# Kernel tuning notes

Hardware: AMD Instinct MI355X
Metric: run time of the kernel (lower is better)

## Reference

```python
import jax, jax.numpy as jnp
import numpy as np

N_NODES = 100000


def gcn_layer(x, src, dst, W, b, num_nodes):
    """PyG GCNConv: out = D^-1/2 (A + I) D^-1/2 (x W) + b, with self-loops."""
    h = x @ W  # [N, out_dim]
    # add self-loops
    loop = jnp.arange(num_nodes, dtype=src.dtype)
    s = jnp.concatenate([src, loop])
    d = jnp.concatenate([dst, loop])
    # symmetric normalization (degree counted on destination, incl. self-loops)
    deg = jax.ops.segment_sum(jnp.ones_like(d, dtype=h.dtype), d, num_segments=num_nodes)
    dinv = jnp.where(deg > 0, jax.lax.rsqrt(deg), 0.0)
    norm = dinv[s] * dinv[d]  # [E+N]
    # gather -> weight -> scatter-add
    msg = h[s] * norm[:, None]  # [E+N, out_dim]
    out = jax.ops.segment_sum(msg, d, num_segments=num_nodes)
    return out + b


def setup_inputs() -> dict:
    key = jax.random.key(0)
    k1, k2, k3, k4 = jax.random.split(key, 4)
    in_chan, h1, h2 = 256, 128, 64
    n_edges = 1600000
    x = jax.random.normal(k1, (N_NODES, in_chan), dtype=jnp.float32)
    edge_index = jax.random.randint(k2, (2, n_edges), 0, N_NODES, dtype=jnp.int64)
    W1 = jax.random.normal(k3, (in_chan, h1), dtype=jnp.float32) * (1.0 / np.sqrt(in_chan))
    b1 = jnp.zeros((h1,), dtype=jnp.float32)
    W2 = jax.random.normal(k4, (h1, h2), dtype=jnp.float32) * (1.0 / np.sqrt(h1))
    b2 = jnp.zeros((h2,), dtype=jnp.float32)
    return {"x": x, "edge_index": edge_index, "W1": W1, "b1": b1, "W2": W2, "b2": b2}


def reference(x, edge_index, W1, b1, W2, b2):
    src, dst = edge_index[0], edge_index[1]
    h = jax.nn.relu(gcn_layer(x, src, dst, W1, b1, N_NODES))
    return jax.nn.relu(gcn_layer(h, src, dst, W2, b2, N_NODES))
```

## Files before the change

kernel.cpp:

```cpp
#include <hip/hip_runtime.h>
#include <hip/hip_fp16.h>

#define NNODES 100000

#define OFF_W1TH     0UL
#define OFF_W1TL     65536UL
#define OFF_W2TH     131072UL
#define OFF_W2TL     147456UL
#define OFF_BCNT     163840UL
#define OFF_BBASE    165888UL
#define OFF_BCUR     167936UL
#define OFF_ROWPTR   400128UL
#define OFF_DINV     1200640UL
#define OFF_COL      1605632UL
#define OFF_EBUF     8005632UL
#define OFF_H1G      8005632UL
#define OFF_H1OUT    59205632UL

typedef __attribute__((ext_vector_type(8))) short bf16x8;
typedef __attribute__((ext_vector_type(4))) float f32x4;

__device__ inline ushort f2bf(float f) {
    unsigned u = __float_as_uint(f);
    unsigned r = u + 0x7fffu + ((u >> 16) & 1u);
    return (ushort)(r >> 16);
}
__device__ inline float bf2f(ushort h) { return __uint_as_float(((unsigned)h) << 16); }

__global__ __launch_bounds__(256) void bincount(const int* __restrict__ dst,
                                                int* __restrict__ bcnt, int E) {
    __shared__ int lc[512];
    int t = threadIdx.x;
    lc[t] = 0; lc[t + 256] = 0;
    __syncthreads();
    for (int e = blockIdx.x * 256 + t; e < E; e += gridDim.x * 256)
        atomicAdd(&lc[dst[e] >> 8], 1);
    __syncthreads();
    if (lc[t]) atomicAdd(&bcnt[t], lc[t]);
    if (lc[t + 256]) atomicAdd(&bcnt[t + 256], lc[t + 256]);
}

__global__ __launch_bounds__(512) void bscan(const int* __restrict__ bcnt,
                                             int* __restrict__ bbase,
                                             int* __restrict__ bcur,
                                             int* __restrict__ rowptr,
                                             int NB, int N, int E) {
    __shared__ int s[512];
    int t = threadIdx.x;
    int v = (t < NB) ? bcnt[t] : 0;
    s[t] = v;
    __syncthreads();
    for (int off = 1; off < 512; off <<= 1) {
        int add = (t >= off) ? s[t - off] : 0;
        __syncthreads();
        s[t] += add;
        __syncthreads();
    }
    if (t < NB) {
        int ex = s[t] - v;
        bbase[t] = ex;
        bcur[t] = ex;
    }
    if (t == 0) rowptr[N] = E;
}

#define CHUNK 4096
__global__ __launch_bounds__(256) void binscatter(const int* __restrict__ src,
                                                  const int* __restrict__ dst,
                                                  int* __restrict__ bcur,
                                                  int2* __restrict__ ebuf, int E) {
    __shared__ int lc[512];
    __shared__ int gb[512];
    int t = threadIdx.x;
    lc[t] = 0; lc[t + 256] = 0;
    __syncthreads();
    int base = blockIdx.x * CHUNK;
    int rb[16];
#pragma unroll
    for (int i = 0; i < 16; ++i) {
        int e = base + i * 256 + t;
        if (e < E) {
            int b = dst[e] >> 8;
            rb[i] = (b << 12) | atomicAdd(&lc[b], 1);
        } else rb[i] = -1;
    }
    __syncthreads();
    if (lc[t]) gb[t] = atomicAdd(&bcur[t], lc[t]);
    if (lc[t + 256]) gb[t + 256] = atomicAdd(&bcur[t + 256], lc[t + 256]);
    __syncthreads();
#pragma unroll
    for (int i = 0; i < 16; ++i) {
        if (rb[i] >= 0) {
            int e = base + i * 256 + t;
            int b = rb[i] >> 12, r = rb[i] & 4095;
            ebuf[gb[b] + r] = make_int2(src[e], dst[e]);
        }
    }
}

__global__ __launch_bounds__(256) void buildcsr(const int2* __restrict__ ebuf,
                                                const int* __restrict__ bbase,
                                                const int* __restrict__ bcnt,
                                                int* __restrict__ rowptr,
                                                int* __restrict__ colarr,
                                                float* __restrict__ dinv, int N) {
    int b = blockIdx.x;
    int t = threadIdx.x;
    int start = bbase[b];
    int cnt = bcnt[b];
    int n0 = b << 8;
    __shared__ int nc[256];
    __shared__ int s[256];
    __shared__ int ncur[256];
    nc[t] = 0;
    __syncthreads();
    for (int e = t; e < cnt; e += 256) atomicAdd(&nc[ebuf[start + e].y - n0], 1);
    __syncthreads();
    int own = nc[t];
    s[t] = own;
    __syncthreads();
    for (int off = 1; off < 256; off <<= 1) {
        int add = (t >= off) ? s[t - off] : 0;
        __syncthreads();
        s[t] += add;
        __syncthreads();
    }
    int rowbase = start + s[t] - own;
    if (n0 + t < N) {
        rowptr[n0 + t] = rowbase;
        dinv[n0 + t] = rsqrtf((float)(own + 1));
    }
    ncur[t] = rowbase;
    __syncthreads();
    for (int e = t; e < cnt; e += 256) {
        int2 p = ebuf[start + e];
        int slot = atomicAdd(&ncur[p.y - n0], 1);
        colarr[slot] = p.x;
    }
}

__global__ __launch_bounds__(256) void split_wt(const float* __restrict__ W,
                                                ushort* __restrict__ hi,
                                                ushort* __restrict__ lo,
                                                int K, int N) {
    int idx = blockIdx.x * 256 + threadIdx.x;
    if (idx >= K * N) return;
    int k = idx / N, n = idx - k * N;
    float v = W[idx];
    ushort h = f2bf(v);
    float rest = v - bf2f(h);
    hi[(size_t)n * K + k] = h;
    lo[(size_t)n * K + k] = f2bf(rest);
}

template <int BN, int KTOT>
__global__ __launch_bounds__(256) void gemm_mfma(const float* __restrict__ A,
                                                 const ushort* __restrict__ Bh_g,
                                                 const ushort* __restrict__ Bl_g,
                                                 const float* __restrict__ dinv,
                                                 _Float16* __restrict__ C, int M) {
    constexpr int KC = 64;
    constexpr int LDK = KC + 8;
    __shared__ ushort Ah[128][LDK];
    __shared__ ushort Al[128][LDK];
    __shared__ ushort Bh[BN][LDK];
    __shared__ ushort Bl[BN][LDK];

    const int tid = threadIdx.x;
    const int wave = tid >> 6;
    const int lane = tid & 63;
    const int lm = lane & 15;
    const int q = lane >> 4;
    const int m0 = blockIdx.x * 128;

    constexpr int NT = BN / 16;
    f32x4 acc[2][NT];
#pragma unroll
    for (int a = 0; a < 2; ++a)
#pragma unroll
        for (int b = 0; b < NT; ++b) acc[a][b] = (f32x4){0.f, 0.f, 0.f, 0.f};

    for (int k0 = 0; k0 < KTOT; k0 += KC) {
#pragma unroll
        for (int i = 0; i < 8; ++i) {
            int v = tid + i * 256;
            int row = v >> 4;
            int kk = (v & 15) << 2;
            int gr = m0 + row;
            float4 val = make_float4(0.f, 0.f, 0.f, 0.f);
            if (gr < M) val = *(const float4*)&A[(size_t)gr * KTOT + k0 + kk];
            ushort h0 = f2bf(val.x), h1 = f2bf(val.y), h2 = f2bf(val.z), h3 = f2bf(val.w);
            *(ushort4*)&Ah[row][kk] = make_ushort4(h0, h1, h2, h3);
            *(ushort4*)&Al[row][kk] = make_ushort4(
                f2bf(val.x - bf2f(h0)), f2bf(val.y - bf2f(h1)),
                f2bf(val.z - bf2f(h2)), f2bf(val.w - bf2f(h3)));
        }
        constexpr int BV = BN * KC / 8 / 256;
#pragma unroll
        for (int i = 0; i < BV; ++i) {
            int v = tid + i * 256;
            int row = v >> 3;
            int kk = (v & 7) << 3;
            *(uint4*)&Bh[row][kk] = *(const uint4*)&Bh_g[(size_t)row * KTOT + k0 + kk];
            *(uint4*)&Bl[row][kk] = *(const uint4*)&Bl_g[(size_t)row * KTOT + k0 + kk];
        }
        __syncthreads();

#pragma unroll
        for (int ks = 0; ks < KC / 32; ++ks) {
            int kb = ks * 32 + q * 8;
            bf16x8 a_h[2], a_l[2];
#pragma unroll
            for (int mt = 0; mt < 2; ++mt) {
                int r = wave * 32 + mt * 16 + lm;
                a_h[mt] = *(const bf16x8*)&Ah[r][kb];
                a_l[mt] = *(const bf16x8*)&Al[r][kb];
            }
#pragma unroll
            for (int nt = 0; nt < NT; ++nt) {
                int c = nt * 16 + lm;
                bf16x8 b_h = *(const bf16x8*)&Bh[c][kb];
                bf16x8 b_l = *(const bf16x8*)&Bl[c][kb];
#pragma unroll
                for (int mt = 0; mt < 2; ++mt) {
                    acc[mt][nt] = __builtin_amdgcn_mfma_f32_16x16x32_bf16(a_h[mt], b_h, acc[mt][nt], 0, 0, 0);
                    acc[mt][nt] = __builtin_amdgcn_mfma_f32_16x16x32_bf16(a_h[mt], b_l, acc[mt][nt], 0, 0, 0);
                    acc[mt][nt] = __builtin_amdgcn_mfma_f32_16x16x32_bf16(a_l[mt], b_h, acc[mt][nt], 0, 0, 0);
                }
            }
        }
        __syncthreads();
    }

#pragma unroll
    for (int mt = 0; mt < 2; ++mt) {
#pragma unroll
        for (int i = 0; i < 4; ++i) {
            int r = m0 + wave * 32 + mt * 16 + q * 4 + i;
            if (r < M) {
                float dv = dinv[r];
#pragma unroll
                for (int nt = 0; nt < NT; ++nt) {
                    C[(size_t)r * BN + nt * 16 + lm] = (_Float16)(acc[mt][nt][i] * dv);
                }
            }
        }
    }
}

__global__ __launch_bounds__(256) void agg_f2h(const __half2* __restrict__ g,
                                               const int* __restrict__ rowptr,
                                               const int* __restrict__ colarr,
                                               const float* __restrict__ dinv,
                                               const float* __restrict__ bias,
                                               float2* __restrict__ out, int n) {
    int node = blockIdx.x * 4 + (threadIdx.x >> 6);
    int lane = threadIdx.x & 63;
    if (node >= n) return;
    int beg = rowptr[node];
    int end = rowptr[node + 1];
    float2 acc = __half22float2(g[(size_t)node * 64 + lane]);
    int p = beg;
    for (; p + 4 <= end; p += 4) {
        int s0 = colarr[p], s1 = colarr[p + 1], s2 = colarr[p + 2], s3 = colarr[p + 3];
        float2 v0 = __half22float2(g[(size_t)s0 * 64 + lane]);
        float2 v1 = __half22float2(g[(size_t)s1 * 64 + lane]);
        float2 v2 = __half22float2(g[(size_t)s2 * 64 + lane]);
        float2 v3 = __half22float2(g[(size_t)s3 * 64 + lane]);
        acc.x += (v0.x + v1.x) + (v2.x + v3.x);
        acc.y += (v0.y + v1.y) + (v2.y + v3.y);
    }
    for (; p < end; ++p) {
        float2 v = __half22float2(g[(size_t)colarr[p] * 64 + lane]);
        acc.x += v.x;
        acc.y += v.y;
    }
    float dv = dinv[node];
    float2 b = ((const float2*)bias)[lane];
    float2 o;
    o.x = fmaxf(fmaf(acc.x, dv, b.x), 0.f);
    o.y = fmaxf(fmaf(acc.y, dv, b.y), 0.f);
    out[(size_t)node * 64 + lane] = o;
}

__global__ __launch_bounds__(256) void agg_f1h(const _Float16* __restrict__ g,
                                               const int* __restrict__ rowptr,
                                               const int* __restrict__ colarr,
                                               const float* __restrict__ dinv,
                                               const float* __restrict__ bias,
                                               float* __restrict__ out, int n) {
    int node = blockIdx.x * 4 + (threadIdx.x >> 6);
    int lane = threadIdx.x & 63;
    if (node >= n) return;
    int beg = rowptr[node];
    int end = rowptr[node + 1];
    float acc = (float)g[(size_t)node * 64 + lane];
    int p = beg;
    for (; p + 4 <= end; p += 4) {
        int s0 = colarr[p], s1 = colarr[p + 1], s2 = colarr[p + 2], s3 = colarr[p + 3];
        float v0 = (float)g[(size_t)s0 * 64 + lane];
        float v1 = (float)g[(size_t)s1 * 64 + lane];
        float v2 = (float)g[(size_t)s2 * 64 + lane];
        float v3 = (float)g[(size_t)s3 * 64 + lane];
        acc += (v0 + v1) + (v2 + v3);
    }
    for (; p < end; ++p) acc += (float)g[(size_t)colarr[p] * 64 + lane];
    float dv = dinv[node];
    float o = fmaxf(fmaf(acc, dv, bias[lane]), 0.f);
    out[(size_t)node * 64 + lane] = o;
}

extern "C" void kernel_launch(void* const* d_in, const int* in_sizes, int n_in,
                              void* d_out, int out_size, void* d_ws, size_t ws_size,
                              hipStream_t stream) {
    const float* x  = (const float*)d_in[0];
    const int*   ei = (const int*)d_in[1];
    const float* W1 = (const float*)d_in[2];
    const float* b1 = (const float*)d_in[3];
    const float* W2 = (const float*)d_in[4];
    const float* b2 = (const float*)d_in[5];
    float* out = (float*)d_out;

    const int E = in_sizes[1] / 2;
    const int H1 = in_sizes[3];
    const int K1 = in_sizes[2] / H1;
    const int N = in_sizes[0] / K1;
    const int H2 = in_sizes[4] / H1;
    const int* src = ei;
    const int* dst = ei + E;
    const int NB = (N + 255) >> 8;

    char* ws = (char*)d_ws;
    ushort*   w1th   = (ushort*)(ws + OFF_W1TH);
    ushort*   w1tl   = (ushort*)(ws + OFF_W1TL);
    ushort*   w2th   = (ushort*)(ws + OFF_W2TH);
    ushort*   w2tl   = (ushort*)(ws + OFF_W2TL);
    int*      bcnt   = (int*)(ws + OFF_BCNT);
    int*      bbase  = (int*)(ws + OFF_BBASE);
    int*      bcur   = (int*)(ws + OFF_BCUR);
    int*      rowptr = (int*)(ws + OFF_ROWPTR);
    float*    dinv   = (float*)(ws + OFF_DINV);
    int*      colarr = (int*)(ws + OFF_COL);
    int2*     ebuf   = (int2*)(ws + OFF_EBUF);
    _Float16* h1g    = (_Float16*)(ws + OFF_H1G);
    float*    h1out  = (float*)(ws + OFF_H1OUT);
    _Float16* h2g    = (_Float16*)(ws + OFF_H1G);

    hipMemsetAsync(bcnt, 0, 512 * sizeof(int), stream);
    bincount<<<256, 256, 0, stream>>>(dst, bcnt, E);
    bscan<<<1, 512, 0, stream>>>(bcnt, bbase, bcur, rowptr, NB, N, E);
    binscatter<<<(E + CHUNK - 1) / CHUNK, 256, 0, stream>>>(src, dst, bcur, ebuf, E);
    buildcsr<<<NB, 256, 0, stream>>>(ebuf, bbase, bcnt, rowptr, colarr, dinv, N);

    split_wt<<<(K1 * H1 + 255) / 256, 256, 0, stream>>>(W1, w1th, w1tl, K1, H1);
    split_wt<<<(H1 * H2 + 255) / 256, 256, 0, stream>>>(W2, w2th, w2tl, H1, H2);

    gemm_mfma<128, 256><<<(N + 127) / 128, 256, 0, stream>>>(x, w1th, w1tl, dinv, h1g, N);
    agg_f2h<<<(N + 3) / 4, 256, 0, stream>>>((const __half2*)h1g, rowptr, colarr, dinv, b1,
                                             (float2*)h1out, N);

    gemm_mfma<64, 128><<<(N + 127) / 128, 256, 0, stream>>>(h1out, w2th, w2tl, dinv, h2g, N);
    agg_f1h<<<(N + 3) / 4, 256, 0, stream>>>(h2g, rowptr, colarr, dinv, b2, out, N);
}
```

Before: 444.9 us.

## Register-prefetch next K-chunk in split-bf16 MFMA GEMM and use truncation split

The GEMM now loads the next K chunk of A and the split weights into registers while MFMAs run on the current chunk held in LDS. This software-pipelines global loads against compute. The K chunk shrinks from 64 to 32, which cuts LDS use, and launch bounds now request 3 blocks per SM to raise occupancy. The hi/lo bf16 split now truncates by bit masking instead of rounding, which is cheaper but changes the residual rounding slightly.

```diff
diff --git a/kernel.cpp b/kernel.cpp
--- a/kernel.cpp
+++ b/kernel.cpp
@@ -26,6 +26,13 @@
     return (ushort)(r >> 16);
 }
 __device__ inline float bf2f(ushort h) { return __uint_as_float(((unsigned)h) << 16); }
+
+__device__ inline unsigned pack_hi(float a, float b) {
+    return (__float_as_uint(a) >> 16) | (__float_as_uint(b) & 0xFFFF0000u);
+}
+__device__ inline float zlow(float a) {
+    return __uint_as_float(__float_as_uint(a) & 0xFFFF0000u);
+}
 
 __global__ __launch_bounds__(256) void bincount(const int* __restrict__ dst,
                                                 int* __restrict__ bcnt, int E) {
@@ -154,12 +161,12 @@
 }
 
 template <int BN, int KTOT>
-__global__ __launch_bounds__(256) void gemm_mfma(const float* __restrict__ A,
-                                                 const ushort* __restrict__ Bh_g,
-                                                 const ushort* __restrict__ Bl_g,
-                                                 const float* __restrict__ dinv,
-                                                 _Float16* __restrict__ C, int M) {
-    constexpr int KC = 64;
+__global__ __launch_bounds__(256, 3) void gemm_mfma(const float* __restrict__ A,
+                                                    const ushort* __restrict__ Bh_g,
+                                                    const ushort* __restrict__ Bl_g,
+                                                    const float* __restrict__ dinv,
+                                                    _Float16* __restrict__ C, int M) {
+    constexpr int KC = 32;
     constexpr int LDK = KC + 8;
     __shared__ ushort Ah[128][LDK];
     __shared__ ushort Al[128][LDK];
@@ -174,59 +181,87 @@
     const int m0 = blockIdx.x * 128;
 
     constexpr int NT = BN / 16;
+    constexpr int BV = BN * KC / 8 / 256;
+
     f32x4 acc[2][NT];
 #pragma unroll
     for (int a = 0; a < 2; ++a)
 #pragma unroll
         for (int b = 0; b < NT; ++b) acc[a][b] = (f32x4){0.f, 0.f, 0.f, 0.f};
 
-    for (int k0 = 0; k0 < KTOT; k0 += KC) {
-#pragma unroll
-        for (int i = 0; i < 8; ++i) {
+    float4 areg[4];
+    uint4 bhreg[BV], blreg[BV];
+
+    auto load_chunk = [&](int k0) {
+#pragma unroll
+        for (int i = 0; i < 4; ++i) {
             int v = tid + i * 256;
-            int row = v >> 4;
-            int kk = (v & 15) << 2;
+            int row = v >> 3;
+            int kk = (v & 7) << 2;
             int gr = m0 + row;
-            float4 val = make_float4(0.f, 0.f, 0.f, 0.f);
-            if (gr < M) val = *(const float4*)&A[(size_t)gr * KTOT + k0 + kk];
-            ushort h0 = f2bf(val.x), h1 = f2bf(val.y), h2 = f2bf(val.z), h3 = f2bf(val.w);
-            *(ushort4*)&Ah[row][kk] = make_ushort4(h0, h1, h2, h3);
-            *(ushort4*)&Al[row][kk] = make_ushort4(
-                f2bf(val.x - bf2f(h0)), f2bf(val.y - bf2f(h1)),
-                f2bf(val.z - bf2f(h2)), f2bf(val.w - bf2f(h3)));
-        }
-        constexpr int BV = BN * KC / 8 / 256;
+            areg[i] = make_float4(0.f, 0.f, 0.f, 0.f);
+            if (gr < M) areg[i] = *(const float4*)&A[(size_t)gr * KTOT + k0 + kk];
+        }
 #pragma unroll
         for (int i = 0; i < BV; ++i) {
             int v = tid + i * 256;
+            int row = v >> 2;
+            int kk = (v & 3) << 3;
+            bhreg[i] = *(const uint4*)&Bh_g[(size_t)row * KTOT + k0 + kk];
+            blreg[i] = *(const uint4*)&Bl_g[(size_t)row * KTOT + k0 + kk];
+        }
+    };
+
+    auto stage_lds = [&]() {
+#pragma unroll
+        for (int i = 0; i < 4; ++i) {
+            int v = tid + i * 256;
             int row = v >> 3;
-            int kk = (v & 7) << 3;
-            *(uint4*)&Bh[row][kk] = *(const uint4*)&Bh_g[(size_t)row * KTOT + k0 + kk];
-            *(uint4*)&Bl[row][kk] = *(const uint4*)&Bl_g[(size_t)row * KTOT + k0 + kk];
-        }
-        __syncthreads();
-
-#pragma unroll
-        for (int ks = 0; ks < KC / 32; ++ks) {
-            int kb = ks * 32 + q * 8;
-            bf16x8 a_h[2], a_l[2];
+            int kk = (v & 7) << 2;
+            float4 val = areg[i];
+            unsigned h01 = pack_hi(val.x, val.y);
+            unsigned h23 = pack_hi(val.z, val.w);
+            float r0 = val.x - zlow(val.x), r1 = val.y - zlow(val.y);
+            float r2 = val.z - zlow(val.z), r3 = val.w - zlow(val.w);
+            unsigned l01 = pack_hi(r0, r1);
+            unsigned l23 = pack_hi(r2, r3);
+            *(uint2*)&Ah[row][kk] = make_uint2(h01, h23);
+            *(uint2*)&Al[row][kk] = make_uint2(l01, l23);
+        }
+#pragma unroll
+        for (int i = 0; i < BV; ++i) {
+            int v = tid + i * 256;
+            int row = v >> 2;
+            int kk = (v & 3) << 3;
+            *(uint4*)&Bh[row][kk] = bhreg[i];
+            *(uint4*)&Bl[row][kk] = blreg[i];
+        }
+    };
+
+    load_chunk(0);
+    for (int k0 = 0; k0 < KTOT; k0 += KC) {
+        stage_lds();
+        __syncthreads();
+        if (k0 + KC < KTOT) load_chunk(k0 + KC);
+
+        int kb = q * 8;
+        bf16x8 a_h[2], a_l[2];
+#pragma unroll
+        for (int mt = 0; mt < 2; ++mt) {
+            int r = wave * 32 + mt * 16 + lm;
+            a_h[mt] = *(const bf16x8*)&Ah[r][kb];
+            a_l[mt] = *(const bf16x8*)&Al[r][kb];
+        }
+#pragma unroll
+        for (int nt = 0; nt < NT; ++nt) {
+            int c = nt * 16 + lm;
+            bf16x8 b_h = *(const bf16x8*)&Bh[c][kb];
+            bf16x8 b_l = *(const bf16x8*)&Bl[c][kb];
 #pragma unroll
             for (int mt = 0; mt < 2; ++mt) {
-                int r = wave * 32 + mt * 16 + lm;
-                a_h[mt] = *(const bf16x8*)&Ah[r][kb];
-                a_l[mt] = *(const bf16x8*)&Al[r][kb];
-            }
-#pragma unroll
-            for (int nt = 0; nt < NT; ++nt) {
-                int c = nt * 16 + lm;
-                bf16x8 b_h = *(const bf16x8*)&Bh[c][kb];
-                bf16x8 b_l = *(const bf16x8*)&Bl[c][kb];
-#pragma unroll
-                for (int mt = 0; mt < 2; ++mt) {
-                    acc[mt][nt] = __builtin_amdgcn_mfma_f32_16x16x32_bf16(a_h[mt], b_h, acc[mt][nt], 0, 0, 0);
-                    acc[mt][nt] = __builtin_amdgcn_mfma_f32_16x16x32_bf16(a_h[mt], b_l, acc[mt][nt], 0, 0, 0);
-                    acc[mt][nt] = __builtin_amdgcn_mfma_f32_16x16x32_bf16(a_l[mt], b_h, acc[mt][nt], 0, 0, 0);
-                }
+                acc[mt][nt] = __builtin_amdgcn_mfma_f32_16x16x32_bf16(a_h[mt], b_h, acc[mt][nt], 0, 0, 0);
+                acc[mt][nt] = __builtin_amdgcn_mfma_f32_16x16x32_bf16(a_h[mt], b_l, acc[mt][nt], 0, 0, 0);
+                acc[mt][nt] = __builtin_amdgcn_mfma_f32_16x16x32_bf16(a_l[mt], b_h, acc[mt][nt], 0, 0, 0);
             }
         }
         __syncthreads();
```

Result: no change. 451.2 us (+1.4%).

## Switch GEMMs to fp16 two-term MFMA with fragment-packed weights and fp16 hidden activations

Applied to the files above, without the earlier changes.

Replaces the bf16 hi/lo split GEMM (three MFMAs per tile) with fp16 MFMAs, where A is rounded to a single fp16 and only the weights keep a hi/lo split, so two MFMAs are issued instead of three. Weights are pre-packed into MFMA fragment order and loaded straight into LDS with global_load_lds, and the layer-1 aggregation output is stored as fp16, which halves the bytes the second GEMM reads. Launch bounds now request 3 blocks per CU. The cost is precision: A loses its low-order correction and the hidden activations pass through fp16, which could push error past tolerance.

```diff
diff --git a/kernel.cpp b/kernel.cpp
--- a/kernel.cpp
+++ b/kernel.cpp
@@ -17,15 +17,14 @@
 #define OFF_H1G      8005632UL
 #define OFF_H1OUT    59205632UL
 
-typedef __attribute__((ext_vector_type(8))) short bf16x8;
+typedef __attribute__((ext_vector_type(8))) _Float16 f16x8;
 typedef __attribute__((ext_vector_type(4))) float f32x4;
 
-__device__ inline ushort f2bf(float f) {
-    unsigned u = __float_as_uint(f);
-    unsigned r = u + 0x7fffu + ((u >> 16) & 1u);
-    return (ushort)(r >> 16);
-}
-__device__ inline float bf2f(ushort h) { return __uint_as_float(((unsigned)h) << 16); }
+__device__ __forceinline__ void async_copy16(void* lds, const void* g) {
+    __builtin_amdgcn_global_load_lds(
+        (const __attribute__((address_space(1))) unsigned*)g,
+        (__attribute__((address_space(3))) unsigned*)lds, 16, 0, 0);
+}
 
 __global__ __launch_bounds__(256) void bincount(const int* __restrict__ dst,
                                                 int* __restrict__ bcnt, int E) {
@@ -139,32 +138,37 @@
     }
 }
 
-__global__ __launch_bounds__(256) void split_wt(const float* __restrict__ W,
-                                                ushort* __restrict__ hi,
-                                                ushort* __restrict__ lo,
-                                                int K, int N) {
+__global__ __launch_bounds__(256) void split_wt_frag(const float* __restrict__ W,
+                                                     _Float16* __restrict__ hi,
+                                                     _Float16* __restrict__ lo,
+                                                     int K, int N) {
     int idx = blockIdx.x * 256 + threadIdx.x;
     if (idx >= K * N) return;
-    int k = idx / N, n = idx - k * N;
-    float v = W[idx];
-    ushort h = f2bf(v);
-    float rest = v - bf2f(h);
-    hi[(size_t)n * K + k] = h;
-    lo[(size_t)n * K + k] = f2bf(rest);
-}
-
-template <int BN, int KTOT>
-__global__ __launch_bounds__(256) void gemm_mfma(const float* __restrict__ A,
-                                                 const ushort* __restrict__ Bh_g,
-                                                 const ushort* __restrict__ Bl_g,
-                                                 const float* __restrict__ dinv,
-                                                 _Float16* __restrict__ C, int M) {
-    constexpr int KC = 64;
-    constexpr int LDK = KC + 8;
-    __shared__ ushort Ah[128][LDK];
-    __shared__ ushort Al[128][LDK];
-    __shared__ ushort Bh[BN][LDK];
-    __shared__ ushort Bl[BN][LDK];
+    int NT = N >> 4;
+    int j = idx & 7;
+    int l = (idx >> 3) & 63;
+    int f = idx >> 9;
+    int nt = f % NT;
+    int kc = f / NT;
+    int k = kc * 32 + (l >> 4) * 8 + j;
+    int n = nt * 16 + (l & 15);
+    float v = W[k * N + n];
+    _Float16 h = (_Float16)v;
+    hi[idx] = h;
+    lo[idx] = (_Float16)(v - (float)h);
+}
+
+template <int BN, int KTOT, bool AFP16>
+__global__ __launch_bounds__(256, 3) void gemm_f16(const void* __restrict__ Araw,
+                                                   const _Float16* __restrict__ Bh_g,
+                                                   const _Float16* __restrict__ Bl_g,
+                                                   const float* __restrict__ dinv,
+                                                   _Float16* __restrict__ C, int M) {
+    constexpr int NT = BN / 16;
+    constexpr int FPW = (2 * NT) / 4;
+    __shared__ _Float16 Ah[128][72];
+    __shared__ _Float16 Bsh[2 * NT * 512];
+    __shared__ _Float16 Bsl[2 * NT * 512];
 
     const int tid = threadIdx.x;
     const int wave = tid >> 6;
@@ -173,59 +177,65 @@
     const int q = lane >> 4;
     const int m0 = blockIdx.x * 128;
 
-    constexpr int NT = BN / 16;
     f32x4 acc[2][NT];
 #pragma unroll
     for (int a = 0; a < 2; ++a)
 #pragma unroll
         for (int b = 0; b < NT; ++b) acc[a][b] = (f32x4){0.f, 0.f, 0.f, 0.f};
 
-    for (int k0 = 0; k0 < KTOT; k0 += KC) {
-#pragma unroll
-        for (int i = 0; i < 8; ++i) {
-            int v = tid + i * 256;
-            int row = v >> 4;
-            int kk = (v & 15) << 2;
+    for (int k0 = 0; k0 < KTOT; k0 += 64) {
+        const int kc0 = k0 >> 5;
+        const _Float16* bh_base = Bh_g + (size_t)kc0 * NT * 512;
+        const _Float16* bl_base = Bl_g + (size_t)kc0 * NT * 512;
+#pragma unroll
+        for (int i = 0; i < FPW; ++i) {
+            int f = wave * FPW + i;
+            async_copy16(&Bsh[f * 512 + lane * 8], bh_base + f * 512 + lane * 8);
+            async_copy16(&Bsl[f * 512 + lane * 8], bl_base + f * 512 + lane * 8);
+        }
+#pragma unroll
+        for (int i = 0; i < 4; ++i) {
+            int flat = tid + i * 256;
+            int row = flat >> 3;
+            int kk = (flat & 7) << 3;
             int gr = m0 + row;
-            float4 val = make_float4(0.f, 0.f, 0.f, 0.f);
-            if (gr < M) val = *(const float4*)&A[(size_t)gr * KTOT + k0 + kk];
-            ushort h0 = f2bf(val.x), h1 = f2bf(val.y), h2 = f2bf(val.z), h3 = f2bf(val.w);
-            *(ushort4*)&Ah[row][kk] = make_ushort4(h0, h1, h2, h3);
-            *(ushort4*)&Al[row][kk] = make_ushort4(
-                f2bf(val.x - bf2f(h0)), f2bf(val.y - bf2f(h1)),
-                f2bf(val.z - bf2f(h2)), f2bf(val.w - bf2f(h3)));
-        }
-        constexpr int BV = BN * KC / 8 / 256;
-#pragma unroll
-        for (int i = 0; i < BV; ++i) {
-            int v = tid + i * 256;
-            int row = v >> 3;
-            int kk = (v & 7) << 3;
-            *(uint4*)&Bh[row][kk] = *(const uint4*)&Bh_g[(size_t)row * KTOT + k0 + kk];
-            *(uint4*)&Bl[row][kk] = *(const uint4*)&Bl_g[(size_t)row * KTOT + k0 + kk];
-        }
-        __syncthreads();
-
-#pragma unroll
-        for (int ks = 0; ks < KC / 32; ++ks) {
-            int kb = ks * 32 + q * 8;
-            bf16x8 a_h[2], a_l[2];
-#pragma unroll
-            for (int mt = 0; mt < 2; ++mt) {
-                int r = wave * 32 + mt * 16 + lm;
-                a_h[mt] = *(const bf16x8*)&Ah[r][kb];
-                a_l[mt] = *(const bf16x8*)&Al[r][kb];
+            if (AFP16) {
+                uint4 hv = make_uint4(0u, 0u, 0u, 0u);
+                if (gr < M)
+                    hv = *(const uint4*)&((const _Float16*)Araw)[(size_t)gr * KTOT + k0 + kk];
+                *(uint4*)&Ah[row][kk] = hv;
+            } else {
+                const float* Af = (const float*)Araw;
+                float4 v0 = make_float4(0.f, 0.f, 0.f, 0.f);
+                float4 v1 = make_float4(0.f, 0.f, 0.f, 0.f);
+                if (gr < M) {
+                    v0 = *(const float4*)&Af[(size_t)gr * KTOT + k0 + kk];
+                    v1 = *(const float4*)&Af[(size_t)gr * KTOT + k0 + kk + 4];
+                }
+                f16x8 h;
+                h[0] = (_Float16)v0.x; h[1] = (_Float16)v0.y;
+                h[2] = (_Float16)v0.z; h[3] = (_Float16)v0.w;
+                h[4] = (_Float16)v1.x; h[5] = (_Float16)v1.y;
+                h[6] = (_Float16)v1.z; h[7] = (_Float16)v1.w;
+                *(f16x8*)&Ah[row][kk] = h;
             }
+        }
+        __syncthreads();
+
+#pragma unroll
+        for (int dkc = 0; dkc < 2; ++dkc) {
+            f16x8 a[2];
+#pragma unroll
+            for (int mt = 0; mt < 2; ++mt)
+                a[mt] = *(const f16x8*)&Ah[wave * 32 + mt * 16 + lm][dkc * 32 + q * 8];
 #pragma unroll
             for (int nt = 0; nt < NT; ++nt) {
-                int c = nt * 16 + lm;
-                bf16x8 b_h = *(const bf16x8*)&Bh[c][kb];
-                bf16x8 b_l = *(const bf16x8*)&Bl[c][kb];
+                f16x8 bh = *(const f16x8*)&Bsh[(dkc * NT + nt) * 512 + lane * 8];
+                f16x8 bl = *(const f16x8*)&Bsl[(dkc * NT + nt) * 512 + lane * 8];
 #pragma unroll
                 for (int mt = 0; mt < 2; ++mt) {
-                    acc[mt][nt] = __builtin_amdgcn_mfma_f32_16x16x32_bf16(a_h[mt], b_h, acc[mt][nt], 0, 0, 0);
-                    acc[mt][nt] = __builtin_amdgcn_mfma_f32_16x16x32_bf16(a_h[mt], b_l, acc[mt][nt], 0, 0, 0);
-                    acc[mt][nt] = __builtin_amdgcn_mfma_f32_16x16x32_bf16(a_l[mt], b_h, acc[mt][nt], 0, 0, 0);
+                    acc[mt][nt] = __builtin_amdgcn_mfma_f32_16x16x32_f16(a[mt], bh, acc[mt][nt], 0, 0, 0);
+                    acc[mt][nt] = __builtin_amdgcn_mfma_f32_16x16x32_f16(a[mt], bl, acc[mt][nt], 0, 0, 0);
                 }
             }
         }
@@ -253,7 +263,7 @@
                                                const int* __restrict__ colarr,
                                                const float* __restrict__ dinv,
                                                const float* __restrict__ bias,
-                                               float2* __restrict__ out, int n) {
+                                               __half2* __restrict__ out, int n) {
     int node = blockIdx.x * 4 + (threadIdx.x >> 6);
     int lane = threadIdx.x & 63;
     if (node >= n) return;
@@ -277,10 +287,9 @@
     }
     float dv = dinv[node];
     float2 b = ((const float2*)bias)[lane];
-    float2 o;
-    o.x = fmaxf(fmaf(acc.x, dv, b.x), 0.f);
-    o.y = fmaxf(fmaf(acc.y, dv, b.y), 0.f);
-    out[(size_t)node * 64 + lane] = o;
+    float ox = fmaxf(fmaf(acc.x, dv, b.x), 0.f);
+    float oy = fmaxf(fmaf(acc.y, dv, b.y), 0.f);
+    out[(size_t)node * 64 + lane] = __floats2half2_rn(ox, oy);
 }
 
 __global__ __launch_bounds__(256) void agg_f1h(const _Float16* __restrict__ g,
@@ -331,10 +340,10 @@
     const int NB = (N + 255) >> 8;
 
     char* ws = (char*)d_ws;
-    ushort*   w1th   = (ushort*)(ws + OFF_W1TH);
-    ushort*   w1tl   = (ushort*)(ws + OFF_W1TL);
-    ushort*   w2th   = (ushort*)(ws + OFF_W2TH);
-    ushort*   w2tl   = (ushort*)(ws + OFF_W2TL);
+    _Float16* w1th   = (_Float16*)(ws + OFF_W1TH);
+    _Float16* w1tl   = (_Float16*)(ws + OFF_W1TL);
+    _Float16* w2th   = (_Float16*)(ws + OFF_W2TH);
+    _Float16* w2tl   = (_Float16*)(ws + OFF_W2TL);
     int*      bcnt   = (int*)(ws + OFF_BCNT);
     int*      bbase  = (int*)(ws + OFF_BBASE);
     int*      bcur   = (int*)(ws + OFF_BCUR);
@@ -343,7 +352,7 @@
     int*      colarr = (int*)(ws + OFF_COL);
     int2*     ebuf   = (int2*)(ws + OFF_EBUF);
     _Float16* h1g    = (_Float16*)(ws + OFF_H1G);
-    float*    h1out  = (float*)(ws + OFF_H1OUT);
+    _Float16* h1out  = (_Float16*)(ws + OFF_H1OUT);
     _Float16* h2g    = (_Float16*)(ws + OFF_H1G);
 
     hipMemsetAsync(bcnt, 0, 512 * sizeof(int), stream);
@@ -352,13 +361,13 @@
     binscatter<<<(E + CHUNK - 1) / CHUNK, 256, 0, stream>>>(src, dst, bcur, ebuf, E);
     buildcsr<<<NB, 256, 0, stream>>>(ebuf, bbase, bcnt, rowptr, colarr, dinv, N);
 
-    split_wt<<<(K1 * H1 + 255) / 256, 256, 0, stream>>>(W1, w1th, w1tl, K1, H1);
-    split_wt<<<(H1 * H2 + 255) / 256, 256, 0, stream>>>(W2, w2th, w2tl, H1, H2);
-
-    gemm_mfma<128, 256><<<(N + 127) / 128, 256, 0, stream>>>(x, w1th, w1tl, dinv, h1g, N);
+    split_wt_frag<<<(K1 * H1 + 255) / 256, 256, 0, stream>>>(W1, w1th, w1tl, K1, H1);
+    split_wt_frag<<<(H1 * H2 + 255) / 256, 256, 0, stream>>>(W2, w2th, w2tl, H1, H2);
+
+    gemm_f16<128, 256, false><<<(N + 127) / 128, 256, 0, stream>>>(x, w1th, w1tl, dinv, h1g, N);
     agg_f2h<<<(N + 3) / 4, 256, 0, stream>>>((const __half2*)h1g, rowptr, colarr, dinv, b1,
-                                             (float2*)h1out, N);
-
-    gemm_mfma<64, 128><<<(N + 127) / 128, 256, 0, stream>>>(h1out, w2th, w2tl, dinv, h2g, N);
+                                             (__half2*)h1out, N);
+
+    gemm_f16<64, 128, true><<<(N + 127) / 128, 256, 0, stream>>>(h1out, w2th, w2tl, dinv, h2g, N);
     agg_f1h<<<(N + 3) / 4, 256, 0, stream>>>(h2g, rowptr, colarr, dinv, b2, out, N);
 }
```

New measurement: 409.6 us. 1.09x faster.
